# Kernel optimization log

Measured on AMD Instinct MI355X. Metric: run time of the kernel, lower is better.

## Reference

```python
import jax, jax.numpy as jnp
import numpy as np

IN_CHANNELS = (256, 512)
SPATIAL = ((64, 64), (32, 32))
BATCH = 4
CORR = 5          # corr_size (patch_size of spatial_correlation_sample)
SEQ = 4           # gating_seq_len
PAD = (CORR - 1) // 2


def conv3x3(x, w, b):
    # NCHW conv, 3x3, stride 1, pad 1 (== padding='SAME')
    y = jax.lax.conv_general_dilated(x, w, (1, 1), 'SAME',
                                     dimension_numbers=('NCHW', 'OIHW', 'NCHW'))
    return y + b[None, :, None, None]


def align(feat2, feat1):
    # spatial_correlation_sample(feat2, feat1, kernel_size=1, patch_size=CORR,
    # padding=0, dilation_patch=1): corr[b,i,j,y,x] = sum_c feat2[b,c,y,x] *
    # feat1[b,c,y+i-PAD,x+j-PAD] (zero outside). Then softmax over the 25
    # offsets with scale 20/corr.max(), then the unrolled shifted-slice warp.
    b, c, h, w = feat1.shape
    pad1 = jnp.pad(feat1, ((0, 0), (0, 0), (PAD, PAD), (PAD, PAD)))
    corr = jnp.stack(
        [jnp.einsum('bchw,bchw->bhw', feat2, pad1[:, :, i:i + h, j:j + w])
         for i in range(CORR) for j in range(CORR)], axis=1)  # [b, 25, h, w]
    # note: any constant channel-normalization of the correlation cancels in
    # the 20/corr.max() scaling, so plain channel-sum is faithful.
    att = jax.nn.softmax(corr * (20.0 / corr.max()), axis=1)
    new = jnp.zeros_like(feat1)
    k = 0
    for i in range(CORR):
        for j in range(CORR):
            new = new + att[:, k:k + 1] * pad1[:, :, i:i + h, j:j + w]
            k += 1
    return new


def level_forward(frames, Wg, bg, Wd, bd, Wc, bc):
    # frames: list of SEQ feature maps [b,C,h,w]; key frame is frames[SEQ-1]
    key_f = frames[SEQ - 1]
    gated = []
    for s in range(SEQ - 1):
        new = align(key_f, frames[s])
        feat = jnp.concatenate([key_f, new], axis=1)           # [b, 2C, h, w]
        g = jax.nn.sigmoid(conv3x3(feat, Wg[s], bg[s]))        # [b, 2, h, w]
        fg = jnp.concatenate([key_f * g[:, 0:1], new * g[:, 1:2]], axis=1)
        gated.append(jax.nn.relu(conv3x3(fg, Wd[s], bd[s])))   # [b, C, h, w]
    total = jnp.concatenate(gated, axis=1)                     # [b, 3C, h, w]
    return jax.nn.relu(conv3x3(total, Wc, bc))


def setup_inputs() -> dict:
    key = jax.random.key(0)
    ks = iter(jax.random.split(key, 64))
    inp = {}
    for s in range(SEQ):
        for l, (c, (h, w)) in enumerate(zip(IN_CHANNELS, SPATIAL)):
            inp[f"x{s}{l}"] = jax.random.normal(next(ks), (BATCH, c, h, w), jnp.float32) * 0.1
    for l, c in enumerate(IN_CHANNELS):
        fan = float(1.0 / np.sqrt(2 * c * 9))
        inp[f"Wg{l}"] = jax.random.uniform(next(ks), (SEQ - 1, 2, 2 * c, 3, 3), jnp.float32, -fan, fan)
        inp[f"bg{l}"] = jnp.zeros((SEQ - 1, 2), jnp.float32)
        inp[f"Wd{l}"] = jax.random.uniform(next(ks), (SEQ - 1, c, 2 * c, 3, 3), jnp.float32, -fan, fan)
        inp[f"bd{l}"] = jnp.zeros((SEQ - 1, c), jnp.float32)
        fan3 = float(1.0 / np.sqrt(3 * c * 9))
        inp[f"Wc{l}"] = jax.random.uniform(next(ks), (c, 3 * c, 3, 3), jnp.float32, -fan3, fan3)
        inp[f"bc{l}"] = jnp.zeros((c,), jnp.float32)
    return inp


def reference(x00, x01, x10, x11, x20, x21, x30, x31,
              Wg0, bg0, Wd0, bd0, Wc0, bc0,
              Wg1, bg1, Wd1, bd1, Wc1, bc1):
    out0 = level_forward([x00, x10, x20, x30], Wg0, bg0, Wd0, bd0, Wc0, bc0)
    out1 = level_forward([x01, x11, x21, x31], Wg1, bg1, Wd1, bd1, Wc1, bc1)
    return (out0, out1)
```

## Files before the change

kernel.cpp:

```cpp
#include <hip/hip_runtime.h>
#include <hip/hip_bf16.h>
#include <math.h>

#define PAD 2

typedef __attribute__((ext_vector_type(8))) short s8v;
typedef __attribute__((ext_vector_type(4))) float f4v;

__device__ __forceinline__ f4v mfma16(s8v a, s8v b, f4v c){
    return __builtin_amdgcn_mfma_f32_16x16x32_bf16(a, b, c, 0, 0, 0);
}

__device__ __forceinline__ unsigned short f2bf(float f){
    unsigned u = __float_as_uint(f);
    unsigned r = u + 0x7FFFu + ((u >> 16) & 1u);
    return (unsigned short)(r >> 16);
}

__device__ __forceinline__ unsigned f2o(float f){
    unsigned b = __float_as_uint(f);
    return (b & 0x80000000u) ? ~b : (b | 0x80000000u);
}
__device__ __forceinline__ float o2f(unsigned u){
    return __uint_as_float((u & 0x80000000u) ? (u & 0x7fffffffu) : ~u);
}

__device__ __forceinline__ float bperm(int adr, float v){
    return __uint_as_float((unsigned)__builtin_amdgcn_ds_bpermute(adr, (int)__float_as_uint(v)));
}

__global__ __launch_bounds__(256)
void corr_v2(const float* __restrict__ key, const float* __restrict__ frame,
             float* __restrict__ corr,
             int C, int CW, int H, int W, int logHW, int logW){
    const int tid = threadIdx.x, lane = tid & 63, wv = tid >> 6;
    const int HW = 1 << logHW;
    const int p0 = blockIdx.x * 64;
    const int b  = p0 >> logHW;
    const int remL = (p0 & (HW - 1)) + lane;
    const int y = remL >> logW, x = remL & (W - 1);

    float m[25];
    #pragma unroll
    for (int t = 0; t < 25; t++){
        const int dy = t / 5 - 2, dx = t % 5 - 2;
        m[t] = (((unsigned)(y + dy) < (unsigned)H) &&
                ((unsigned)(x + dx) < (unsigned)W)) ? 1.f : 0.f;
    }
    int adr[4];
    const int dxs[4] = {-2, -1, 1, 2};
    #pragma unroll
    for (int i = 0; i < 4; i++) adr[i] = ((lane + dxs[i]) & 63) << 2;

    int roff[5];
    #pragma unroll
    for (int r = 0; r < 5; r++){
        const int dy = r - 2;
        roff[r] = ((unsigned)(y + dy) < (unsigned)H) ? dy * W : 0;
    }

    const int c0 = (blockIdx.y * 4 + wv) * CW;
    const float* kp = key   + (((size_t)b * C + c0) << logHW) + remL;
    const float* fp = frame + (((size_t)b * C + c0) << logHW) + remL;

    float acc[25];
    #pragma unroll
    for (int t = 0; t < 25; t++) acc[t] = 0.f;

    for (int ci = 0; ci < CW; ci++){
        const float k = kp[0];
        float f[5];
        #pragma unroll
        for (int r = 0; r < 5; r++) f[r] = fp[roff[r]];
        #pragma unroll
        for (int r = 0; r < 5; r++){
            float v[5];
            v[0] = bperm(adr[0], f[r]);
            v[1] = bperm(adr[1], f[r]);
            v[2] = f[r];
            v[3] = bperm(adr[2], f[r]);
            v[4] = bperm(adr[3], f[r]);
            #pragma unroll
            for (int j = 0; j < 5; j++)
                acc[r * 5 + j] += k * (v[j] * m[r * 5 + j]);
        }
        kp += HW; fp += HW;
    }

    __shared__ float sacc[4][25][64];
    #pragma unroll
    for (int t = 0; t < 25; t++) sacc[wv][t][lane] = acc[t];
    __syncthreads();
    #pragma unroll
    for (int tg = 0; tg < 7; tg++){
        const int t = wv + tg * 4;
        if (t < 25){
            const float s = sacc[0][t][lane] + sacc[1][t][lane] +
                            sacc[2][t][lane] + sacc[3][t][lane];
            atomicAdd(corr + (((size_t)b * 25 + t) << logHW) + remL, s);
        }
    }
}

__global__ void max_kernel(const float* __restrict__ corr, unsigned* __restrict__ gmax){
    float v = corr[(size_t)blockIdx.x * 256 + threadIdx.x];
    #pragma unroll
    for (int o = 32; o > 0; o >>= 1) v = fmaxf(v, __shfl_down(v, o));
    if ((threadIdx.x & 63) == 0) atomicMax(gmax, f2o(v));
}

__global__ void att_kernel(float* __restrict__ corr, const unsigned* __restrict__ gmax,
                           int logHW){
    const int p = blockIdx.x * 256 + threadIdx.x;
    const int b = p >> logHW;
    const int rem = p & ((1 << logHW) - 1);
    float* cp = corr + (((size_t)b * 25) << logHW) + rem;
    const float scale = 20.f / o2f(*gmax);

    float z[25]; float m = -INFINITY;
    #pragma unroll
    for (int k = 0; k < 25; k++){
        z[k] = cp[k << logHW] * scale;
        m = fmaxf(m, z[k]);
    }
    float s = 0.f;
    #pragma unroll
    for (int k = 0; k < 25; k++){ z[k] = expf(z[k] - m); s += z[k]; }
    const float inv = 1.f / s;
    #pragma unroll
    for (int k = 0; k < 25; k++) cp[k << logHW] = z[k] * inv;
}

__global__ __launch_bounds__(256)
void warp_v2(const float* __restrict__ frame, const float* __restrict__ att,
             float* __restrict__ newf,
             int C, int CW, int H, int W, int logHW, int logW){
    const int tid = threadIdx.x, lane = tid & 63, wv = tid >> 6;
    const int HW = 1 << logHW;
    const int p0 = blockIdx.x * 64;
    const int b  = p0 >> logHW;
    const int remL = (p0 & (HW - 1)) + lane;
    const int y = remL >> logW, x = remL & (W - 1);

    int adr[4];
    const int dxs[4] = {-2, -1, 1, 2};
    #pragma unroll
    for (int i = 0; i < 4; i++) adr[i] = ((lane + dxs[i]) & 63) << 2;

    int roff[5];
    #pragma unroll
    for (int r = 0; r < 5; r++){
        const int dy = r - 2;
        roff[r] = ((unsigned)(y + dy) < (unsigned)H) ? dy * W : 0;
    }

    const float* ap = att + (((size_t)b * 25) << logHW) + remL;
    float a[25];
    #pragma unroll
    for (int t = 0; t < 25; t++){
        const int dy = t / 5 - 2, dx = t % 5 - 2;
        const float mk = (((unsigned)(y + dy) < (unsigned)H) &&
                          ((unsigned)(x + dx) < (unsigned)W)) ? 1.f : 0.f;
        a[t] = ap[(size_t)t << logHW] * mk;
    }

    const int c0 = (blockIdx.y * 4 + wv) * CW;
    const float* fp = frame + (((size_t)b * C + c0) << logHW) + remL;
    float*       op = newf  + (((size_t)b * C + c0) << logHW) + remL;

    for (int ci = 0; ci < CW; ci++){
        float f[5];
        #pragma unroll
        for (int r = 0; r < 5; r++) f[r] = fp[roff[r]];
        float acc = 0.f;
        #pragma unroll
        for (int r = 0; r < 5; r++){
            float v[5];
            v[0] = bperm(adr[0], f[r]);
            v[1] = bperm(adr[1], f[r]);
            v[2] = f[r];
            v[3] = bperm(adr[2], f[r]);
            v[4] = bperm(adr[3], f[r]);
            #pragma unroll
            for (int j = 0; j < 5; j++)
                acc += a[r * 5 + j] * v[j];
        }
        op[0] = acc;
        fp += HW; op += HW;
    }
}

__global__ __launch_bounds__(256)
void gate_v2(const float* __restrict__ key, const float* __restrict__ newf,
             const float* __restrict__ Wg, float* __restrict__ gz,
             int C, int CW, int H, int W, int logHW, int logW){
    const int tid = threadIdx.x, lane = tid & 63, wv = tid >> 6;
    const int HW = 1 << logHW;
    const int p0 = blockIdx.x * 64;
    const int b  = p0 >> logHW;
    const int remL = (p0 & (HW - 1)) + lane;
    const int y = remL >> logW, x = remL & (W - 1);

    float m[9];
    #pragma unroll
    for (int t = 0; t < 9; t++){
        const int dy = t / 3 - 1, dx = t % 3 - 1;
        m[t] = (((unsigned)(y + dy) < (unsigned)H) &&
                ((unsigned)(x + dx) < (unsigned)W)) ? 1.f : 0.f;
    }
    const int adrL = ((lane - 1) & 63) << 2;
    const int adrR = ((lane + 1) & 63) << 2;

    int roff[3];
    #pragma unroll
    for (int r = 0; r < 3; r++){
        const int dy = r - 1;
        roff[r] = ((unsigned)(y + dy) < (unsigned)H) ? dy * W : 0;
    }

    const int c0 = (blockIdx.y * 4 + wv) * CW;
    const float* base = (c0 < C)
        ? key  + (((size_t)b * C + c0)       << logHW)
        : newf + (((size_t)b * C + (c0 - C)) << logHW);
    const float* ip = base + remL;

    float z0 = 0.f, z1 = 0.f;
    for (int ci = 0; ci < CW; ci++){
        const int u = c0 + ci;
        const float* w0 = Wg + (size_t)u * 9;
        const float* w1 = Wg + ((size_t)2 * C + u) * 9;
        float f[3];
        #pragma unroll
        for (int r = 0; r < 3; r++) f[r] = ip[roff[r]];
        #pragma unroll
        for (int r = 0; r < 3; r++){
            float v[3];
            v[0] = bperm(adrL, f[r]);
            v[1] = f[r];
            v[2] = bperm(adrR, f[r]);
            #pragma unroll
            for (int j = 0; j < 3; j++){
                const float val = v[j] * m[r * 3 + j];
                z0 += val * w0[r * 3 + j];
                z1 += val * w1[r * 3 + j];
            }
        }
        ip += HW;
    }

    __shared__ float sz[2][4][64];
    sz[0][wv][lane] = z0; sz[1][wv][lane] = z1;
    __syncthreads();
    if (wv < 2){
        const float s = sz[wv][0][lane] + sz[wv][1][lane] +
                        sz[wv][2][lane] + sz[wv][3][lane];
        atomicAdd(gz + ((size_t)b * 2 + wv) * HW + remL, s);
    }
}

__global__ void prep_gin(const float* __restrict__ key, const float* __restrict__ newf,
                         const float* __restrict__ g, const float* __restrict__ bg,
                         unsigned short* __restrict__ gin,
                         int C, int HW){
    __shared__ unsigned short tile[64][65];
    int tid = threadIdx.x;
    int pt0 = blockIdx.x * 64;
    int u0  = blockIdx.y * 64;
    int b   = pt0 / HW;
    int rem0 = pt0 - b * HW;
    const float* gb = g + (size_t)(b * 2) * HW;

    #pragma unroll
    for (int it = 0; it < 16; it++){
        int idx = it * 256 + tid;
        int ur = idx >> 6, pc = idx & 63;
        int u = u0 + ur; int rem = rem0 + pc;
        const float* src; int sel;
        if (u < C){ src = key  + ((size_t)b * C + u) * HW;       sel = 0; }
        else      { src = newf + ((size_t)b * C + (u - C)) * HW; sel = 1; }
        float zz = gb[(size_t)sel * HW + rem] + bg[sel];
        float gv = 1.f / (1.f + expf(-zz));
        float v = src[rem] * gv;
        tile[ur][pc] = f2bf(v);
    }
    __syncthreads();
    unsigned short* go = gin + (size_t)pt0 * (2 * C) + u0;
    #pragma unroll
    for (int it = 0; it < 16; it++){
        int idx = it * 256 + tid;
        int pr = idx >> 6, uc = idx & 63;
        go[(size_t)pr * (2 * C) + uc] = tile[uc][pr];
    }
}

__global__ void prep_w(const float* __restrict__ W, unsigned short* __restrict__ Wt,
                       int Cin){
    int ci = blockIdx.y * 256 + threadIdx.x;
    int bx = blockIdx.x;
    int co = bx / 9, t = bx - co * 9;
    Wt[(size_t)bx * Cin + ci] = f2bf(W[((size_t)co * Cin + ci) * 9 + t]);
}

template<int BN, int EPI>
__global__ __launch_bounds__(256, 2)
void conv_mfma(const unsigned short* __restrict__ gin,
               const unsigned short* __restrict__ Wt,
               const float* __restrict__ bias,
               unsigned short* __restrict__ obf, int ostride,
               float* __restrict__ of32,
               const void* __restrict__ zp,
               int Cin, int Cout, int H, int W, int logHW, int logW)
{
    constexpr int BM = 64;
    constexpr int BNh = BN / 2;
    constexpr int NJ = BN / 32;
    __shared__ __align__(16) unsigned short sA[2][BM * 32];
    __shared__ __align__(16) unsigned short sB[2][BN * 32];

    const int tid = threadIdx.x;
    const int lane = tid & 63;
    const int wv = tid >> 6;
    const int wm = wv >> 1, wn = wv & 1;
    const int ln = lane & 15, q = lane >> 4;

    const int p0 = blockIdx.x * BM;
    const int b  = p0 >> logHW;
    const int rem0 = p0 - (b << logHW);

    const int rowA0 = tid >> 2;
    const int gc8 = ((tid & 3) ^ ((tid >> 3) & 3)) * 8;
    const int remA0 = rem0 + rowA0;
    const int yA0 = remA0 >> logW, xA0 = remA0 & (W - 1);
    const size_t pbase = ((size_t)b << logHW);

    const int nt0 = blockIdx.y * BN;
    const size_t Ktot = (size_t)9 * Cin;
    const unsigned short* wB0 = Wt + (size_t)(nt0 + rowA0) * Ktot + gc8;

    f4v acc[2][NJ];
    #pragma unroll
    for (int i = 0; i < 2; i++)
        #pragma unroll
        for (int j = 0; j < NJ; j++){ f4v z = {0.f, 0.f, 0.f, 0.f}; acc[i][j] = z; }

    const int cblocks = Cin >> 5;
    const int total = 9 * cblocks;

    int scb = 0;
    int st  = 0;
    bool sv = (yA0 > 0) && (xA0 > 0);
    const unsigned short* sa  = gin + (pbase + remA0 + (-W - 1)) * Cin + gc8;
    const unsigned short* swb = wB0;

    struct Regs { f4v a, b0, b1; };
    Regs R0, R1;

    auto issue = [&](Regs& r){
        r.a  = *(const f4v*)(sv ? (const void*)(sa + scb * 32) : zp);
        r.b0 = *(const f4v*)swb;
        if constexpr (BN == 128) r.b1 = *(const f4v*)(swb + (size_t)64 * Ktot);
        swb += 32;
        if (++scb == cblocks){
            scb = 0; ++st;
            const int dy = st / 3 - 1, dx = st - (st / 3) * 3 - 1;
            sv = ((unsigned)(yA0 + dy) < (unsigned)H) && ((unsigned)(xA0 + dx) < (unsigned)W);
            sa = gin + (pbase + remA0 + dy * W + dx) * Cin + gc8;
        }
    };
    auto commit = [&](const Regs& r, int bsel){
        *(f4v*)((char*)sA[bsel] + (size_t)tid * 16) = r.a;
        char* dB = (char*)sB[bsel];
        *(f4v*)(dB + (size_t)tid * 16) = r.b0;
        if constexpr (BN == 128) *(f4v*)(dB + 4096 + (size_t)tid * 16) = r.b1;
    };

    const int rchunk = (q ^ ((ln >> 1) & 3)) * 8;
    auto compute = [&](int bsel){
        const unsigned short* A = sA[bsel];
        const unsigned short* B = sB[bsel];
        s8v af[2];
        #pragma unroll
        for (int i = 0; i < 2; i++)
            af[i] = *(const s8v*)(A + (wm * 32 + i * 16 + ln) * 32 + rchunk);
        __builtin_amdgcn_s_setprio(1);
        #pragma unroll
        for (int j = 0; j < NJ; j++){
            s8v bfr = *(const s8v*)(B + (wn * BNh + j * 16 + ln) * 32 + rchunk);
            #pragma unroll
            for (int i = 0; i < 2; i++)
                acc[i][j] = mfma16(af[i], bfr, acc[i][j]);
        }
        __builtin_amdgcn_s_setprio(0);
    };

    #define WAIT_CUR()  do{ if constexpr (BN == 128) asm volatile("s_waitcnt vmcnt(3)" ::: "memory"); \
                            else                     asm volatile("s_waitcnt vmcnt(2)" ::: "memory"); }while(0)
    #define WAIT_ALL()  asm volatile("s_waitcnt vmcnt(0)" ::: "memory")

    issue(R0); issue(R1);

    for (int kb = 0; kb < total; kb += 2){
        if (kb + 1 < total) WAIT_CUR(); else WAIT_ALL();
        __builtin_amdgcn_sched_barrier(0);
        commit(R0, 0);
        if (kb + 2 < total) issue(R0);
        asm volatile("s_waitcnt lgkmcnt(0)" ::: "memory");
        __builtin_amdgcn_sched_barrier(0);
        __builtin_amdgcn_s_barrier();
        compute(0);

        const int kb1 = kb + 1;
        if (kb1 + 1 < total) WAIT_CUR(); else WAIT_ALL();
        __builtin_amdgcn_sched_barrier(0);
        commit(R1, 1);
        if (kb1 + 2 < total) issue(R1);
        asm volatile("s_waitcnt lgkmcnt(0)" ::: "memory");
        __builtin_amdgcn_sched_barrier(0);
        __builtin_amdgcn_s_barrier();
        compute(1);
    }
    #undef WAIT_CUR
    #undef WAIT_ALL

    #pragma unroll
    for (int i = 0; i < 2; i++){
        const int m0 = wm * 32 + i * 16 + q * 4;
        const int p = p0 + m0;
        #pragma unroll
        for (int j = 0; j < NJ; j++){
            const int n = nt0 + wn * BNh + j * 16 + ln;
            const float bv = bias[n];
            if (EPI == 0){
                #pragma unroll
                for (int r = 0; r < 4; r++){
                    float v = fmaxf(acc[i][j][r] + bv, 0.f);
                    obf[(size_t)(p + r) * ostride + n] = f2bf(v);
                }
            } else {
                f4v o;
                #pragma unroll
                for (int r = 0; r < 4; r++) o[r] = fmaxf(acc[i][j][r] + bv, 0.f);
                const int rem = rem0 + m0;
                *(f4v*)(of32 + (((size_t)b * Cout + n) << logHW) + rem) = o;
            }
        }
    }
}

extern "C" void kernel_launch(void* const* d_in, const int* in_sizes, int n_in,
                              void* d_out, int out_size, void* d_ws, size_t ws_size,
                              hipStream_t stream){
    (void)in_sizes; (void)n_in; (void)out_size; (void)ws_size;

    const float* X[4][2];
    for (int s = 0; s < 4; s++)
        for (int l = 0; l < 2; l++)
            X[s][l] = (const float*)d_in[s * 2 + l];
    const float* Wg[2] = { (const float*)d_in[8],  (const float*)d_in[14] };
    const float* bg[2] = { (const float*)d_in[9],  (const float*)d_in[15] };
    const float* Wd[2] = { (const float*)d_in[10], (const float*)d_in[16] };
    const float* bd[2] = { (const float*)d_in[11], (const float*)d_in[17] };
    const float* Wc[2] = { (const float*)d_in[12], (const float*)d_in[18] };
    const float* bc[2] = { (const float*)d_in[13], (const float*)d_in[19] };
    float* out = (float*)d_out;

    char* ws = (char*)d_ws;
    unsigned* gmax = (unsigned*)ws;
    const void* zp = (const void*)(ws + 1024);
    float* corrbuf = (float*)(ws + 4096);
    float* newbuf  = (float*)(ws + 4096 + 1638400);
    unsigned short* wtbuf = (unsigned short*)newbuf;
    float* gbuf    = (float*)(ws + 4096 + 1638400 + 16777216);
    unsigned short* ginbuf = (unsigned short*)(ws + 4096 + 1638400 + 16777216 + 131072);
    unsigned short* totbuf = (unsigned short*)(ws + 4096 + 1638400 + 16777216 + 131072 + 16777216);

    hipMemsetAsync(ws, 0, 4096, stream);

    const int Cs[2] = {256, 512};
    const int Hs[2] = {64, 32};
    const int logWs[2] = {6, 5};
    const int logHWs[2] = {12, 10};
    const size_t outOff[2] = {0, (size_t)4 * 256 * 4096};

    for (int l = 0; l < 2; l++){
        const int C = Cs[l], H = Hs[l], W = Hs[l], HW = H * W;
        const int logW = logWs[l], logHW = logHWs[l];
        const float* key = X[3][l];
        const int pblk = 4 * HW / 256;
        const int Mt = 4 * HW / 64;

        const int gx  = 4 * HW / 64;
        const int S   = (l == 0) ? 2 : 8;
        const int CWc = C / (4 * S);
        const int CWg = (2 * C) / (4 * S);

        for (int s = 0; s < 3; s++){
            const float* fr = X[s][l];
            unsigned* slot = gmax + (l * 3 + s);
            hipMemsetAsync(corrbuf, 0, (size_t)4 * 25 * HW * 4, stream);
            hipMemsetAsync(gbuf,    0, (size_t)4 * 2 * HW * 4, stream);
            corr_v2<<<dim3(gx, S), 256, 0, stream>>>(
                key, fr, corrbuf, C, CWc, H, W, logHW, logW);
            max_kernel<<<25 * 4 * HW / 256, 256, 0, stream>>>(corrbuf, slot);
            att_kernel<<<pblk, 256, 0, stream>>>(corrbuf, slot, logHW);
            warp_v2<<<dim3(gx, S), 256, 0, stream>>>(
                fr, corrbuf, newbuf, C, CWc, H, W, logHW, logW);
            gate_v2<<<dim3(gx, S), 256, 0, stream>>>(
                key, newbuf, Wg[l] + (size_t)s * 2 * (2 * C) * 9,
                gbuf, C, CWg, H, W, logHW, logW);
            prep_gin<<<dim3(4 * HW / 64, 2 * C / 64), 256, 0, stream>>>(
                key, newbuf, gbuf, bg[l] + (size_t)s * 2, ginbuf, C, HW);
            prep_w<<<dim3(C * 9, 2 * C / 256), 256, 0, stream>>>(
                Wd[l] + (size_t)s * C * 2 * C * 9, wtbuf, 2 * C);
            if (l == 0)
                conv_mfma<128, 0><<<dim3(Mt, C / 128), 256, 0, stream>>>(
                    ginbuf, wtbuf, bd[l] + s * C, totbuf + s * C, 3 * C,
                    nullptr, zp, 2 * C, C, H, W, logHW, logW);
            else
                conv_mfma<64, 0><<<dim3(Mt, C / 64), 256, 0, stream>>>(
                    ginbuf, wtbuf, bd[l] + s * C, totbuf + s * C, 3 * C,
                    nullptr, zp, 2 * C, C, H, W, logHW, logW);
        }
        prep_w<<<dim3(C * 9, 3 * C / 256), 256, 0, stream>>>(Wc[l], wtbuf, 3 * C);
        if (l == 0)
            conv_mfma<128, 1><<<dim3(Mt, 2), 256, 0, stream>>>(
                totbuf, wtbuf, bc[l], nullptr, 0,
                out + outOff[l], zp, 3 * C, C, H, W, logHW, logW);
        else
            conv_mfma<64, 1><<<dim3(Mt, 8), 256, 0, stream>>>(
                totbuf, wtbuf, bc[l], nullptr, 0,
                out + outOff[l], zp, 3 * C, C, H, W, logHW, logW);
    }
}
```

Before: 1.929 ms.

## Deepen conv MFMA pipeline to four LDS buffers, two k-blocks per barrier

The implicit-GEMM conv kernel now uses four LDS stages and four register staging sets instead of two. Each barrier phase commits and computes two 32-wide k-blocks, which halves the number of workgroup barriers and keeps more global loads in flight. The vmcnt waits are scaled to match the deeper prefetch. In exchange it doubles LDS use per block and raises register pressure from the extra staging registers, which may limit occupancy. It also assumes the k-block count is a multiple of four, which holds for all channel sizes in this task.

```diff
diff --git a/kernel.cpp b/kernel.cpp
--- a/kernel.cpp
+++ b/kernel.cpp
@@ -314,8 +314,8 @@
     constexpr int BM = 64;
     constexpr int BNh = BN / 2;
     constexpr int NJ = BN / 32;
-    __shared__ __align__(16) unsigned short sA[2][BM * 32];
-    __shared__ __align__(16) unsigned short sB[2][BN * 32];
+    __shared__ __align__(16) unsigned short sA[4][BM * 32];
+    __shared__ __align__(16) unsigned short sB[4][BN * 32];
 
     const int tid = threadIdx.x;
     const int lane = tid & 63;
@@ -345,6 +345,7 @@
 
     const int cblocks = Cin >> 5;
     const int total = 9 * cblocks;
+    const int npairs = total >> 1;
 
     int scb = 0;
     int st  = 0;
@@ -353,9 +354,9 @@
     const unsigned short* swb = wB0;
 
     struct Regs { f4v a, b0, b1; };
-    Regs R0, R1;
-
-    auto issue = [&](Regs& r){
+    Regs R0, R1, R2, R3;
+
+    auto issue1 = [&](Regs& r){
         r.a  = *(const f4v*)(sv ? (const void*)(sa + scb * 32) : zp);
         r.b0 = *(const f4v*)swb;
         if constexpr (BN == 128) r.b1 = *(const f4v*)(swb + (size_t)64 * Ktot);
@@ -367,17 +368,17 @@
             sa = gin + (pbase + remA0 + dy * W + dx) * Cin + gc8;
         }
     };
-    auto commit = [&](const Regs& r, int bsel){
-        *(f4v*)((char*)sA[bsel] + (size_t)tid * 16) = r.a;
-        char* dB = (char*)sB[bsel];
+    auto commit1 = [&](const Regs& r, int buf){
+        *(f4v*)((char*)sA[buf] + (size_t)tid * 16) = r.a;
+        char* dB = (char*)sB[buf];
         *(f4v*)(dB + (size_t)tid * 16) = r.b0;
         if constexpr (BN == 128) *(f4v*)(dB + 4096 + (size_t)tid * 16) = r.b1;
     };
 
     const int rchunk = (q ^ ((ln >> 1) & 3)) * 8;
-    auto compute = [&](int bsel){
-        const unsigned short* A = sA[bsel];
-        const unsigned short* B = sB[bsel];
+    auto compute1 = [&](int buf){
+        const unsigned short* A = sA[buf];
+        const unsigned short* B = sB[buf];
         s8v af[2];
         #pragma unroll
         for (int i = 0; i < 2; i++)
@@ -393,31 +394,30 @@
         __builtin_amdgcn_s_setprio(0);
     };
 
-    #define WAIT_CUR()  do{ if constexpr (BN == 128) asm volatile("s_waitcnt vmcnt(3)" ::: "memory"); \
-                            else                     asm volatile("s_waitcnt vmcnt(2)" ::: "memory"); }while(0)
+    #define WAIT_CUR()  do{ if constexpr (BN == 128) asm volatile("s_waitcnt vmcnt(6)" ::: "memory"); \
+                            else                     asm volatile("s_waitcnt vmcnt(4)" ::: "memory"); }while(0)
     #define WAIT_ALL()  asm volatile("s_waitcnt vmcnt(0)" ::: "memory")
 
-    issue(R0); issue(R1);
-
-    for (int kb = 0; kb < total; kb += 2){
-        if (kb + 1 < total) WAIT_CUR(); else WAIT_ALL();
+    issue1(R0); issue1(R1); issue1(R2); issue1(R3);
+
+    for (int t = 0; t < npairs; t += 2){
+        if (t + 1 < npairs) WAIT_CUR(); else WAIT_ALL();
         __builtin_amdgcn_sched_barrier(0);
-        commit(R0, 0);
-        if (kb + 2 < total) issue(R0);
+        commit1(R0, 0); commit1(R1, 1);
+        if (t + 2 < npairs){ issue1(R0); issue1(R1); }
         asm volatile("s_waitcnt lgkmcnt(0)" ::: "memory");
         __builtin_amdgcn_sched_barrier(0);
         __builtin_amdgcn_s_barrier();
-        compute(0);
-
-        const int kb1 = kb + 1;
-        if (kb1 + 1 < total) WAIT_CUR(); else WAIT_ALL();
+        compute1(0); compute1(1);
+
+        if (t + 2 < npairs) WAIT_CUR(); else WAIT_ALL();
         __builtin_amdgcn_sched_barrier(0);
-        commit(R1, 1);
-        if (kb1 + 2 < total) issue(R1);
+        commit1(R2, 2); commit1(R3, 3);
+        if (t + 3 < npairs){ issue1(R2); issue1(R3); }
         asm volatile("s_waitcnt lgkmcnt(0)" ::: "memory");
         __builtin_amdgcn_sched_barrier(0);
         __builtin_amdgcn_s_barrier();
-        compute(1);
+        compute1(2); compute1(3);
     }
     #undef WAIT_CUR
     #undef WAIT_ALL
```

Measured after the change: 1.796 ms. 1.07x faster.
